# Kernel optimization log

Measured on AMD Instinct MI355X. Metric: run time of the kernel, lower is better.

The kernel has to match this reference:

```python
import jax, jax.numpy as jnp
import numpy as np

N, E, D, L = 50000, 1_600_000, 128, 2


def setup_inputs() -> dict:
    key = jax.random.key(0)
    ks = jax.random.split(key, 16)
    scale = 1.0 / np.sqrt(D).astype(np.float32)
    w = lambda k: jax.random.normal(k, (L, D, D), jnp.float32) * scale
    return {
        "x": jax.random.normal(ks[0], (N, D), jnp.float32),
        "edge_index": jax.random.randint(ks[1], (2, E), 0, N),
        "edge_weight": jax.random.uniform(ks[2], (E,), jnp.float32),
        "h": jax.random.normal(ks[3], (L, N, D), jnp.float32),
        "Wxz": w(ks[4]), "bxz": jnp.zeros((L, D), jnp.float32),
        "Whz": w(ks[5]), "bhz": jnp.zeros((L, D), jnp.float32),
        "Wxr": w(ks[6]), "bxr": jnp.zeros((L, D), jnp.float32),
        "Whr": w(ks[7]), "bhr": jnp.zeros((L, D), jnp.float32),
        "Wxh": w(ks[8]), "bxh": jnp.zeros((L, D), jnp.float32),
        "Whh": w(ks[9]), "bhh": jnp.zeros((L, D), jnp.float32),
    }


def reference(x, edge_index, edge_weight, h,
              Wxz, bxz, Whz, bhz, Wxr, bxr, Whr, bhr, Wxh, bxh, Whh, bhh):
    n = x.shape[0]
    # GCN normalization with self-loops (PyG gcn_norm, fill_value=1),
    # shared across all 12 GCNConv calls since edge_index/edge_weight are identical.
    loops = jnp.arange(n)
    row = jnp.concatenate([edge_index[0], loops])  # source
    col = jnp.concatenate([edge_index[1], loops])  # target
    w = jnp.concatenate([edge_weight, jnp.ones((n,), edge_weight.dtype)])
    deg = jax.ops.segment_sum(w, col, num_segments=n)
    dinv = jnp.where(deg > 0, jax.lax.rsqrt(deg), 0.0)
    norm = dinv[row] * w * dinv[col]  # [E+N]

    def conv(xin, W, b):
        xw = xin @ W  # [N, D] linear transform first (PyG GCNConv)
        agg = jax.ops.segment_sum(norm[:, None] * xw[row], col, num_segments=n)
        return agg + b

    h_out = []
    xin = x
    for i in range(h.shape[0]):
        z = jax.nn.sigmoid(conv(xin, Wxz[i], bxz[i]) + conv(h[i], Whz[i], bhz[i]))
        r = jax.nn.sigmoid(conv(xin, Wxr[i], bxr[i]) + conv(h[i], Whr[i], bhr[i]))
        ht = jnp.tanh(conv(xin, Wxh[i], bxh[i]) + conv(r * h[i], Whh[i], bhh[i]))
        ho = z * h[i] + (1 - z) * ht
        h_out.append(ho)
        xin = ho
    return jnp.stack(h_out)  # [L, N, D]
```

## Files before the change

kernel.cpp:

```cpp
#include <hip/hip_runtime.h>
#include <cstdint>

#define D128 128

typedef __attribute__((ext_vector_type(8))) short bf16x8;
typedef __attribute__((ext_vector_type(4))) float f32x4;


static __device__ __forceinline__ unsigned short f2bf(float x) {
  unsigned int u = __float_as_uint(x);
  unsigned int r = (u + 0x7FFFu + ((u >> 16) & 1u)) >> 16;
  return (unsigned short)r;
}
static __device__ __forceinline__ float bf2f(unsigned short h) {
  return __uint_as_float((unsigned int)h << 16);
}
static __device__ __forceinline__ float bf_lo(unsigned int v) {
  return __uint_as_float(v << 16);
}
static __device__ __forceinline__ float bf_hi(unsigned int v) {
  return __uint_as_float(v & 0xFFFF0000u);
}
static __device__ __forceinline__ float sigf(float x) {
  return 1.0f / (1.0f + __expf(-x));
}
static __device__ __forceinline__ bf16x8 lds_load8(const unsigned short* p) {
  union { unsigned long long q[2]; bf16x8 v; } u;
  u.q[0] = *(const unsigned long long*)p;
  u.q[1] = *(const unsigned long long*)(p + 4);
  return u.v;
}

#define FIXSCALE 8388608.0f


__global__ void k_init(unsigned long long* __restrict__ packed, int n) {
  int i = blockIdx.x * blockDim.x + threadIdx.x;
  if (i < n) packed[i] = 0ULL;
}

__global__ void k_passA(const int* __restrict__ ei, const float* __restrict__ ew,
                        unsigned long long* __restrict__ packed,
                        int* __restrict__ rank, int E) {
  int e = blockIdx.x * blockDim.x + threadIdx.x;
  if (e >= E) return;
  int c = ei[E + e];
  unsigned int fw = (unsigned int)(ew[e] * FIXSCALE + 0.5f);
  unsigned long long old =
      atomicAdd(&packed[c], (1ULL << 32) | (unsigned long long)fw);
  rank[e] = (int)(old >> 32);
}

__global__ void k_dinv(const unsigned long long* __restrict__ packed,
                       float* __restrict__ dinv, int n) {
  int i = blockIdx.x * blockDim.x + threadIdx.x;
  if (i < n) {
    float deg = 1.0f + (float)(unsigned int)(packed[i] & 0xFFFFFFFFu) / FIXSCALE;
    dinv[i] = rsqrtf(deg);
  }
}

__global__ void k_scan1(const unsigned long long* __restrict__ packed,
                        int* __restrict__ out, int* __restrict__ bsum, int n) {
  __shared__ int s[256];
  int t = threadIdx.x;
  int base = blockIdx.x * 1024 + t * 4;
  int c0 = (base + 0 < n) ? (int)(packed[base + 0] >> 32) : 0;
  int c1 = (base + 1 < n) ? (int)(packed[base + 1] >> 32) : 0;
  int c2 = (base + 2 < n) ? (int)(packed[base + 2] >> 32) : 0;
  int c3 = (base + 3 < n) ? (int)(packed[base + 3] >> 32) : 0;
  int tot = c0 + c1 + c2 + c3;
  s[t] = tot;
  __syncthreads();
  for (int off = 1; off < 256; off <<= 1) {
    int v = (t >= off) ? s[t - off] : 0;
    __syncthreads();
    s[t] += v;
    __syncthreads();
  }
  int excl = (t == 0) ? 0 : s[t - 1];
  if (base + 0 < n) out[base + 0] = excl;
  if (base + 1 < n) out[base + 1] = excl + c0;
  if (base + 2 < n) out[base + 2] = excl + c0 + c1;
  if (base + 3 < n) out[base + 3] = excl + c0 + c1 + c2;
  if (t == 255) bsum[blockIdx.x] = s[255];
}

__global__ void k_scan2(int* __restrict__ bsum, int nb) {
  __shared__ int s[64];
  int t = threadIdx.x;
  if (t < nb) s[t] = bsum[t];
  __syncthreads();
  if (t == 0) {
    int acc = 0;
    for (int i = 0; i < nb; ++i) { int v = s[i]; s[i] = acc; acc += v; }
  }
  __syncthreads();
  if (t < nb) bsum[t] = s[t];
}

__global__ void k_scan3(int* __restrict__ rowptr, const int* __restrict__ bsum,
                        int n, int E) {
  int i = blockIdx.x * blockDim.x + threadIdx.x;
  if (i < n) rowptr[i] += bsum[i >> 10];
  if (i == 0) rowptr[n] = E;
}

__global__ void k_passB(const int* __restrict__ ei, const float* __restrict__ ew,
                        const float* __restrict__ dinv, const int* __restrict__ rowptr,
                        const int* __restrict__ rank, int2* __restrict__ epk, int E) {
  int e = blockIdx.x * blockDim.x + threadIdx.x;
  if (e >= E) return;
  int r = ei[e];
  int c = ei[E + e];
  int p = rowptr[c] + rank[e];
  float nm = dinv[r] * ew[e];
  epk[p] = make_int2(r, __float_as_int(nm));
}


#define GSTRIDE 44
#define GBUF 5632
#define CSTRIDE 136

__global__ __launch_bounds__(256)
void k_gemm_pair_mfma(const float* __restrict__ A0, const float* __restrict__ A1,
                      const float* __restrict__ B0, const float* __restrict__ B1,
                      unsigned short* __restrict__ C, int cstride, int coff, int nrows) {
  __shared__ unsigned short lds[4 * GBUF];
  unsigned short* Ahi = lds;
  unsigned short* Alo = lds + GBUF;
  unsigned short* Bhi = lds + 2 * GBUF;
  unsigned short* Blo = lds + 3 * GBUF;

  const int t = threadIdx.x;
  const int w = t >> 6;
  const int l = t & 63;
  const int r = l & 15;
  const int g = l >> 4;
  const int wr = (w >> 1) * 64;
  const int wc = (w & 1) * 64;
  const int row0 = blockIdx.x * 128;

  const int sa_row = t >> 1;
  const int sa_k = (t & 1) * 16;
  const int sb_k = (t & 15) * 2;
  const int sb_n = (t >> 4) * 8;

  f32x4 acc[4][4];
  const f32x4 zero4 = {0.0f, 0.0f, 0.0f, 0.0f};
#pragma unroll
  for (int i = 0; i < 4; ++i)
#pragma unroll
    for (int j = 0; j < 4; ++j) acc[i][j] = zero4;

  const float* Ap[2] = {A0, A1};
  const float* Bp[2] = {B0, B1};

  for (int s = 0; s < 2; ++s) {
    const float* A = Ap[s];
    const float* B = Bp[s];
    for (int kt = 0; kt < 128; kt += 32) {
      __syncthreads();
      {
        int grow = row0 + sa_row;
        float v[16];
        if (grow < nrows) {
          const float* ap = &A[(size_t)grow * D128 + kt + sa_k];
#pragma unroll
          for (int q = 0; q < 4; ++q) {
            float4 f = *(const float4*)(ap + q * 4);
            v[q * 4 + 0] = f.x; v[q * 4 + 1] = f.y;
            v[q * 4 + 2] = f.z; v[q * 4 + 3] = f.w;
          }
        } else {
#pragma unroll
          for (int q = 0; q < 16; ++q) v[q] = 0.0f;
        }
        unsigned short hi[16], lo[16];
#pragma unroll
        for (int q = 0; q < 16; ++q) {
          unsigned short hb = f2bf(v[q]);
          hi[q] = hb;
          lo[q] = f2bf(v[q] - bf2f(hb));
        }
        const unsigned long long* hp = (const unsigned long long*)hi;
        const unsigned long long* lp = (const unsigned long long*)lo;
        int off = sa_row * GSTRIDE + sa_k;
#pragma unroll
        for (int q = 0; q < 4; ++q) {
          *(unsigned long long*)&Ahi[off + q * 4] = hp[q];
          *(unsigned long long*)&Alo[off + q * 4] = lp[q];
        }
      }
      {
        const float* bp0 = &B[(size_t)(kt + sb_k) * D128 + sb_n];
        const float* bp1 = bp0 + D128;
        float u0[8], u1[8];
#pragma unroll
        for (int q = 0; q < 2; ++q) {
          float4 f0 = *(const float4*)(bp0 + q * 4);
          float4 f1 = *(const float4*)(bp1 + q * 4);
          u0[q * 4 + 0] = f0.x; u0[q * 4 + 1] = f0.y;
          u0[q * 4 + 2] = f0.z; u0[q * 4 + 3] = f0.w;
          u1[q * 4 + 0] = f1.x; u1[q * 4 + 1] = f1.y;
          u1[q * 4 + 2] = f1.z; u1[q * 4 + 3] = f1.w;
        }
#pragma unroll
        for (int q = 0; q < 8; ++q) {
          unsigned short h0 = f2bf(u0[q]);
          unsigned short h1 = f2bf(u1[q]);
          unsigned short l0 = f2bf(u0[q] - bf2f(h0));
          unsigned short l1 = f2bf(u1[q] - bf2f(h1));
          int off = (sb_n + q) * GSTRIDE + sb_k;
          *(unsigned int*)&Bhi[off] = (unsigned int)h0 | ((unsigned int)h1 << 16);
          *(unsigned int*)&Blo[off] = (unsigned int)l0 | ((unsigned int)l1 << 16);
        }
      }
      __syncthreads();
      bf16x8 afh[4], afl[4], bfh[4], bfl[4];
#pragma unroll
      for (int i = 0; i < 4; ++i) {
        int off = (wr + i * 16 + r) * GSTRIDE + g * 8;
        afh[i] = lds_load8(&Ahi[off]);
        afl[i] = lds_load8(&Alo[off]);
      }
#pragma unroll
      for (int j = 0; j < 4; ++j) {
        int off = (wc + j * 16 + r) * GSTRIDE + g * 8;
        bfh[j] = lds_load8(&Bhi[off]);
        bfl[j] = lds_load8(&Blo[off]);
      }
#pragma unroll
      for (int i = 0; i < 4; ++i)
#pragma unroll
        for (int j = 0; j < 4; ++j) {
          acc[i][j] = __builtin_amdgcn_mfma_f32_16x16x32_bf16(afh[i], bfh[j], acc[i][j], 0, 0, 0);
          acc[i][j] = __builtin_amdgcn_mfma_f32_16x16x32_bf16(afl[i], bfh[j], acc[i][j], 0, 0, 0);
          acc[i][j] = __builtin_amdgcn_mfma_f32_16x16x32_bf16(afh[i], bfl[j], acc[i][j], 0, 0, 0);
        }
    }
  }

  __syncthreads();
#pragma unroll
  for (int i = 0; i < 4; ++i)
#pragma unroll
    for (int j = 0; j < 4; ++j)
#pragma unroll
      for (int q = 0; q < 4; ++q) {
        int rr = wr + i * 16 + g * 4 + q;
        int cc = wc + j * 16 + r;
        lds[rr * CSTRIDE + cc] = f2bf(acc[i][j][q]);
      }
  __syncthreads();
  {
    int orow = row0 + (t >> 1);
    if (orow < nrows) {
      int half = (t & 1) * 64;
      const unsigned short* src = &lds[(t >> 1) * CSTRIDE + half];
      unsigned short* dst = &C[(size_t)orow * cstride + coff + half];
#pragma unroll
      for (int q = 0; q < 8; ++q)
        *(uint4*)(dst + q * 8) = *(const uint4*)(src + q * 8);
    }
  }
}


__global__ __launch_bounds__(256)
void k_agg_act1(const unsigned int* __restrict__ ubf,
                const float* __restrict__ hl,
                const int2* __restrict__ epk,
                const int* __restrict__ rowptr,
                const float* __restrict__ dinv,
                const float* __restrict__ bxz, const float* __restrict__ bhz,
                const float* __restrict__ bxr, const float* __restrict__ bhr,
                float* __restrict__ zbuf, float* __restrict__ rhbuf, int N) {
  __shared__ int2 se[4][64];
  int wv = threadIdx.x >> 6;
  int l = threadIdx.x & 63;
  int n = blockIdx.x * 4 + wv;
  if (n >= N) return;

  float dv = dinv[n];
  const unsigned int* up = ubf + (size_t)n * 128 + l * 2;
  uint2 sv = *(const uint2*)up;
  float a0 = dv * bf_lo(sv.x);
  float a1 = dv * bf_hi(sv.x);
  float a2 = dv * bf_lo(sv.y);
  float a3 = dv * bf_hi(sv.y);

  int e0 = rowptr[n], e1 = rowptr[n + 1];
  for (int base = e0; base < e1; base += 64) {
    int m = min(64, e1 - base);
    if (l < m) se[wv][l] = epk[base + l];
    __builtin_amdgcn_wave_barrier();
#pragma unroll 4
    for (int j = 0; j < m; ++j) {
      int2 e = se[wv][j];
      float nm = __int_as_float(e.y);
      uint2 v = *(const uint2*)(ubf + (size_t)e.x * 128 + l * 2);
      a0 += nm * bf_lo(v.x);
      a1 += nm * bf_hi(v.x);
      a2 += nm * bf_lo(v.y);
      a3 += nm * bf_hi(v.y);
    }
    __builtin_amdgcn_wave_barrier();
  }
  a0 *= dv; a1 *= dv; a2 *= dv; a3 *= dv;

  int c = l * 4;
  if (c < 128) {
    float4 o;
    o.x = sigf(a0 + bxz[c + 0] + bhz[c + 0]);
    o.y = sigf(a1 + bxz[c + 1] + bhz[c + 1]);
    o.z = sigf(a2 + bxz[c + 2] + bhz[c + 2]);
    o.w = sigf(a3 + bxz[c + 3] + bhz[c + 3]);
    *(float4*)&zbuf[(size_t)n * D128 + c] = o;
  } else {
    int cc = c - 128;
    float4 hv = *(const float4*)&hl[(size_t)n * D128 + cc];
    float4 o;
    o.x = sigf(a0 + bxr[cc + 0] + bhr[cc + 0]) * hv.x;
    o.y = sigf(a1 + bxr[cc + 1] + bhr[cc + 1]) * hv.y;
    o.z = sigf(a2 + bxr[cc + 2] + bhr[cc + 2]) * hv.z;
    o.w = sigf(a3 + bxr[cc + 3] + bhr[cc + 3]) * hv.w;
    *(float4*)&rhbuf[(size_t)n * D128 + cc] = o;
  }
}

__global__ __launch_bounds__(256)
void k_agg_act2(const unsigned int* __restrict__ ubf,
                const float* __restrict__ hl,
                const int2* __restrict__ epk,
                const int* __restrict__ rowptr,
                const float* __restrict__ dinv,
                const float* __restrict__ bxh, const float* __restrict__ bhh,
                const float* __restrict__ zbuf,
                float* __restrict__ out, int N) {
  __shared__ int2 se[4][64];
  int wv = threadIdx.x >> 6;
  int l = threadIdx.x & 63;
  int n = blockIdx.x * 4 + wv;
  if (n >= N) return;

  float dv = dinv[n];
  unsigned int sv = ubf[(size_t)n * 64 + l];
  float a0 = dv * bf_lo(sv);
  float a1 = dv * bf_hi(sv);

  int e0 = rowptr[n], e1 = rowptr[n + 1];
  for (int base = e0; base < e1; base += 64) {
    int m = min(64, e1 - base);
    if (l < m) se[wv][l] = epk[base + l];
    __builtin_amdgcn_wave_barrier();
#pragma unroll 4
    for (int j = 0; j < m; ++j) {
      int2 e = se[wv][j];
      float nm = __int_as_float(e.y);
      unsigned int v = ubf[(size_t)e.x * 64 + l];
      a0 += nm * bf_lo(v);
      a1 += nm * bf_hi(v);
    }
    __builtin_amdgcn_wave_barrier();
  }
  a0 *= dv; a1 *= dv;

  int c = l * 2;
  float2 hv = *(const float2*)&hl[(size_t)n * D128 + c];
  float2 zz = *(const float2*)&zbuf[(size_t)n * D128 + c];
  float ht0 = tanhf(a0 + bxh[c + 0] + bhh[c + 0]);
  float ht1 = tanhf(a1 + bxh[c + 1] + bhh[c + 1]);
  float2 o;
  o.x = zz.x * hv.x + (1.0f - zz.x) * ht0;
  o.y = zz.y * hv.y + (1.0f - zz.y) * ht1;
  *(float2*)&out[(size_t)n * D128 + c] = o;
}


static inline char* align16(char* p) {
  return (char*)(((uintptr_t)p + 15) & ~(uintptr_t)15);
}

extern "C" void kernel_launch(void* const* d_in, const int* in_sizes, int n_in,
                              void* d_out, int out_size, void* d_ws, size_t ws_size,
                              hipStream_t stream) {
  const float* x = (const float*)d_in[0];
  const int* ei = (const int*)d_in[1];
  const float* ew = (const float*)d_in[2];
  const float* h = (const float*)d_in[3];
  const float* Wxz = (const float*)d_in[4];
  const float* bxz = (const float*)d_in[5];
  const float* Whz = (const float*)d_in[6];
  const float* bhz = (const float*)d_in[7];
  const float* Wxr = (const float*)d_in[8];
  const float* bxr = (const float*)d_in[9];
  const float* Whr = (const float*)d_in[10];
  const float* bhr = (const float*)d_in[11];
  const float* Wxh = (const float*)d_in[12];
  const float* bxh = (const float*)d_in[13];
  const float* Whh = (const float*)d_in[14];
  const float* bhh = (const float*)d_in[15];
  float* out = (float*)d_out;

  const int N = in_sizes[0] / D128;
  const int E = in_sizes[2];
  const int L = in_sizes[3] / (N * D128);

  char* w = (char*)d_ws;
  unsigned long long* packed = (unsigned long long*)w; w += (size_t)N * 8; w = align16(w);
  float* dinv = (float*)w;  w += (size_t)N * 4;        w = align16(w);
  int* rowptr = (int*)w;    w += (size_t)(N + 1) * 4;  w = align16(w);
  int* bsum = (int*)w;      w += 64 * 4;               w = align16(w);
  int* rank = (int*)w;      w += (size_t)E * 4;        w = align16(w);
  int2* epk = (int2*)w;     w += (size_t)E * 8;        w = align16(w);
  unsigned int* bufA = (unsigned int*)w;
  unsigned short* bufA_h = (unsigned short*)w;
  w += (size_t)N * 256 * 2; w = align16(w);
  float* zbuf = (float*)w;  w += (size_t)N * D128 * 4; w = align16(w);
  float* rhbuf = (float*)w; w += (size_t)N * D128 * 4; w = align16(w);

  int gN = (N + 255) / 256;
  int gE = (E + 255) / 256;
  int nScanBlk = (N + 1023) / 1024;
  int gGemm = (N + 127) / 128;
  int gAgg = (N + 3) / 4;

  k_init<<<gN, 256, 0, stream>>>(packed, N);
  k_passA<<<gE, 256, 0, stream>>>(ei, ew, packed, rank, E);
  k_dinv<<<gN, 256, 0, stream>>>(packed, dinv, N);
  k_scan1<<<nScanBlk, 256, 0, stream>>>(packed, rowptr, bsum, N);
  k_scan2<<<1, 64, 0, stream>>>(bsum, nScanBlk);
  k_scan3<<<gN, 256, 0, stream>>>(rowptr, bsum, N, E);
  k_passB<<<gE, 256, 0, stream>>>(ei, ew, dinv, rowptr, rank, epk, E);

  const float* xin = x;
  for (int l = 0; l < L; ++l) {
    const float* hl = h + (size_t)l * N * D128;
    const float* Wxz_l = Wxz + (size_t)l * D128 * D128;
    const float* Whz_l = Whz + (size_t)l * D128 * D128;
    const float* Wxr_l = Wxr + (size_t)l * D128 * D128;
    const float* Whr_l = Whr + (size_t)l * D128 * D128;
    const float* Wxh_l = Wxh + (size_t)l * D128 * D128;
    const float* Whh_l = Whh + (size_t)l * D128 * D128;
    const float* bxz_l = bxz + (size_t)l * D128;
    const float* bhz_l = bhz + (size_t)l * D128;
    const float* bxr_l = bxr + (size_t)l * D128;
    const float* bhr_l = bhr + (size_t)l * D128;
    const float* bxh_l = bxh + (size_t)l * D128;
    const float* bhh_l = bhh + (size_t)l * D128;

    k_gemm_pair_mfma<<<gGemm, 256, 0, stream>>>(xin, hl, Wxz_l, Whz_l, bufA_h, 256, 0, N);
    k_gemm_pair_mfma<<<gGemm, 256, 0, stream>>>(xin, hl, Wxr_l, Whr_l, bufA_h, 256, 128, N);
    k_agg_act1<<<gAgg, 256, 0, stream>>>(bufA, hl, epk, rowptr, dinv,
                                         bxz_l, bhz_l, bxr_l, bhr_l, zbuf, rhbuf, N);

    k_gemm_pair_mfma<<<gGemm, 256, 0, stream>>>(xin, rhbuf, Wxh_l, Whh_l, bufA_h, 128, 0, N);
    float* ho = out + (size_t)l * N * D128;
    k_agg_act2<<<gAgg, 256, 0, stream>>>(bufA, hl, epk, rowptr, dinv,
                                         bxh_l, bhh_l, zbuf, ho, N);
    xin = ho;
  }
}
```

Before: 850.1 us.

## Quantize z/r gate GEMM outputs to int8 with per-row scales for aggregation

The z and r gate GEMMs now write per-row, per-half int8 values with an fp32 scale instead of bf16. The first aggregation kernel dequantizes on the fly and corrects for the +128 offset using an accumulated weight sum. This halves the bytes gathered per edge in the bandwidth-bound sparse aggregation, but adds a scale load per edge and extra quantization error in the gate pre-activations.

```diff
diff --git a/kernel.cpp b/kernel.cpp
--- a/kernel.cpp
+++ b/kernel.cpp
@@ -123,10 +123,12 @@
 #define GBUF 5632
 #define CSTRIDE 136
 
+template <bool Q>
 __global__ __launch_bounds__(256)
 void k_gemm_pair_mfma(const float* __restrict__ A0, const float* __restrict__ A1,
                       const float* __restrict__ B0, const float* __restrict__ B1,
-                      unsigned short* __restrict__ C, int cstride, int coff, int nrows) {
+                      unsigned short* __restrict__ Cb, unsigned char* __restrict__ Cq,
+                      float* __restrict__ scl, int cstride, int coff, int nrows) {
   __shared__ unsigned short lds[4 * GBUF];
   unsigned short* Ahi = lds;
   unsigned short* Alo = lds + GBUF;
@@ -256,20 +258,54 @@
   __syncthreads();
   {
     int orow = row0 + (t >> 1);
-    if (orow < nrows) {
-      int half = (t & 1) * 64;
-      const unsigned short* src = &lds[(t >> 1) * CSTRIDE + half];
-      unsigned short* dst = &C[(size_t)orow * cstride + coff + half];
-#pragma unroll
-      for (int q = 0; q < 8; ++q)
-        *(uint4*)(dst + q * 8) = *(const uint4*)(src + q * 8);
+    int half = (t & 1) * 64;
+    const unsigned short* src = &lds[(t >> 1) * CSTRIDE + half];
+    if (!Q) {
+      if (orow < nrows) {
+        unsigned short* dst = &Cb[(size_t)orow * cstride + coff + half];
+#pragma unroll
+        for (int q = 0; q < 8; ++q)
+          *(uint4*)(dst + q * 8) = *(const uint4*)(src + q * 8);
+      }
+    } else {
+      const unsigned int* sp = (const unsigned int*)src;
+      float mx = 0.0f;
+#pragma unroll
+      for (int q = 0; q < 32; ++q) {
+        unsigned int v = sp[q];
+        mx = fmaxf(mx, fmaxf(fabsf(bf_lo(v)), fabsf(bf_hi(v))));
+      }
+      mx = fmaxf(mx, __shfl_xor(mx, 1));
+      mx = fmaxf(mx, 1e-12f);
+      float s = mx * (1.0f / 127.0f);
+      float inv = 127.0f / mx;
+      if (orow < nrows) {
+        unsigned int ob[16];
+#pragma unroll
+        for (int q = 0; q < 16; ++q) {
+          unsigned int v0 = sp[q * 2];
+          unsigned int v1 = sp[q * 2 + 1];
+          int q0 = (int)rintf(bf_lo(v0) * inv) + 128;
+          int q1 = (int)rintf(bf_hi(v0) * inv) + 128;
+          int q2 = (int)rintf(bf_lo(v1) * inv) + 128;
+          int q3 = (int)rintf(bf_hi(v1) * inv) + 128;
+          ob[q] = (unsigned int)(q0 & 0xFF) | ((unsigned int)(q1 & 0xFF) << 8) |
+                  ((unsigned int)(q2 & 0xFF) << 16) | ((unsigned int)(q3 & 0xFF) << 24);
+        }
+        unsigned char* dst = Cq + (size_t)orow * cstride + coff + half;
+#pragma unroll
+        for (int q = 0; q < 4; ++q)
+          *(uint4*)(dst + q * 16) = *(const uint4*)&ob[q * 4];
+        if ((t & 1) == 0) scl[orow * 2 + (coff >> 7)] = s;
+      }
     }
   }
 }
 
 
 __global__ __launch_bounds__(256)
-void k_agg_act1(const unsigned int* __restrict__ ubf,
+void k_agg_act1(const unsigned int* __restrict__ uq,
+                const float2* __restrict__ scl,
                 const float* __restrict__ hl,
                 const int2* __restrict__ epk,
                 const int* __restrict__ rowptr,
@@ -284,12 +320,15 @@
   if (n >= N) return;
 
   float dv = dinv[n];
-  const unsigned int* up = ubf + (size_t)n * 128 + l * 2;
-  uint2 sv = *(const uint2*)up;
-  float a0 = dv * bf_lo(sv.x);
-  float a1 = dv * bf_hi(sv.x);
-  float a2 = dv * bf_lo(sv.y);
-  float a3 = dv * bf_hi(sv.y);
+  float2 sn = scl[n];
+  float sself = (l < 32) ? sn.x : sn.y;
+  float w0 = dv * sself;
+  unsigned int bs = uq[(size_t)n * 64 + l];
+  float a0 = w0 * (float)(bs & 0xFF);
+  float a1 = w0 * (float)((bs >> 8) & 0xFF);
+  float a2 = w0 * (float)((bs >> 16) & 0xFF);
+  float a3 = w0 * (float)(bs >> 24);
+  float sumw = w0;
 
   int e0 = rowptr[n], e1 = rowptr[n + 1];
   for (int base = e0; base < e1; base += 64) {
@@ -300,15 +339,22 @@
     for (int j = 0; j < m; ++j) {
       int2 e = se[wv][j];
       float nm = __int_as_float(e.y);
-      uint2 v = *(const uint2*)(ubf + (size_t)e.x * 128 + l * 2);
-      a0 += nm * bf_lo(v.x);
-      a1 += nm * bf_hi(v.x);
-      a2 += nm * bf_lo(v.y);
-      a3 += nm * bf_hi(v.y);
+      float2 s2 = scl[e.x];
+      float ns = nm * ((l < 32) ? s2.x : s2.y);
+      unsigned int v = uq[(size_t)e.x * 64 + l];
+      a0 += ns * (float)(v & 0xFF);
+      a1 += ns * (float)((v >> 8) & 0xFF);
+      a2 += ns * (float)((v >> 16) & 0xFF);
+      a3 += ns * (float)(v >> 24);
+      sumw += ns;
     }
     __builtin_amdgcn_wave_barrier();
   }
-  a0 *= dv; a1 *= dv; a2 *= dv; a3 *= dv;
+  float off = 128.0f * sumw;
+  a0 = (a0 - off) * dv;
+  a1 = (a1 - off) * dv;
+  a2 = (a2 - off) * dv;
+  a3 = (a3 - off) * dv;
 
   int c = l * 4;
   if (c < 128) {
@@ -415,9 +461,13 @@
   int* bsum = (int*)w;      w += 64 * 4;               w = align16(w);
   int* rank = (int*)w;      w += (size_t)E * 4;        w = align16(w);
   int2* epk = (int2*)w;     w += (size_t)E * 8;        w = align16(w);
+  unsigned int* uq = (unsigned int*)w;
+  unsigned char* uq_b = (unsigned char*)w;
+  w += (size_t)N * 256;     w = align16(w);
+  float* sclA = (float*)w;  w += (size_t)N * 8;        w = align16(w);
   unsigned int* bufA = (unsigned int*)w;
   unsigned short* bufA_h = (unsigned short*)w;
-  w += (size_t)N * 256 * 2; w = align16(w);
+  w += (size_t)N * 128 * 2; w = align16(w);
   float* zbuf = (float*)w;  w += (size_t)N * D128 * 4; w = align16(w);
   float* rhbuf = (float*)w; w += (size_t)N * D128 * 4; w = align16(w);
 
@@ -451,12 +501,15 @@
     const float* bxh_l = bxh + (size_t)l * D128;
     const float* bhh_l = bhh + (size_t)l * D128;
 
-    k_gemm_pair_mfma<<<gGemm, 256, 0, stream>>>(xin, hl, Wxz_l, Whz_l, bufA_h, 256, 0, N);
-    k_gemm_pair_mfma<<<gGemm, 256, 0, stream>>>(xin, hl, Wxr_l, Whr_l, bufA_h, 256, 128, N);
-    k_agg_act1<<<gAgg, 256, 0, stream>>>(bufA, hl, epk, rowptr, dinv,
+    k_gemm_pair_mfma<true><<<gGemm, 256, 0, stream>>>(
+        xin, hl, Wxz_l, Whz_l, nullptr, uq_b, sclA, 256, 0, N);
+    k_gemm_pair_mfma<true><<<gGemm, 256, 0, stream>>>(
+        xin, hl, Wxr_l, Whr_l, nullptr, uq_b, sclA, 256, 128, N);
+    k_agg_act1<<<gAgg, 256, 0, stream>>>(uq, (const float2*)sclA, hl, epk, rowptr, dinv,
                                          bxz_l, bhz_l, bxr_l, bhr_l, zbuf, rhbuf, N);
 
-    k_gemm_pair_mfma<<<gGemm, 256, 0, stream>>>(xin, rhbuf, Wxh_l, Whh_l, bufA_h, 128, 0, N);
+    k_gemm_pair_mfma<false><<<gGemm, 256, 0, stream>>>(
+        xin, rhbuf, Wxh_l, Whh_l, bufA_h, nullptr, nullptr, 128, 0, N);
     float* ho = out + (size_t)l * N * D128;
     k_agg_act2<<<gAgg, 256, 0, stream>>>(bufA, hl, epk, rowptr, dinv,
                                          bxh_l, bhh_l, zbuf, ho, N);
```

After: 745.5 us. 12.3% less time.
